# Performance work log

Measured on AMD Instinct MI355X. Metric: run time of the kernel, lower is better.

Reference implementation:

```python
import jax, jax.numpy as jnp
import numpy as np

EMBED_DIM = 1024
NUM_HEADS = 16
HEAD_DIM = EMBED_DIM // NUM_HEADS


def setup_inputs() -> dict:
    key = jax.random.key(0)
    ks = jax.random.split(key, 9)
    B, T, C = 2, 2048, EMBED_DIM
    s = 1.0 / np.sqrt(C)
    return {
        "x": jax.random.normal(ks[0], (B, T, C), dtype=jnp.float32),
        "Wq": jax.random.normal(ks[1], (C, C), dtype=jnp.float32) * s,
        "bq": jnp.zeros((C,), dtype=jnp.float32),
        "Wk": jax.random.normal(ks[2], (C, C), dtype=jnp.float32) * s,
        "bk": jnp.zeros((C,), dtype=jnp.float32),
        "Wv": jax.random.normal(ks[3], (C, C), dtype=jnp.float32) * s,
        "bv": jnp.zeros((C,), dtype=jnp.float32),
        "Wo": jax.random.normal(ks[4], (C, C), dtype=jnp.float32) * s,
        "bo": jnp.zeros((C,), dtype=jnp.float32),
    }


def reference(x, Wq, bq, Wk, bk, Wv, bv, Wo, bo):
    B, T, C = x.shape
    H, D = NUM_HEADS, HEAD_DIM
    # projections (torch Linear: x @ W.T + b; here W stored as [in,out])
    q = (x @ Wq + bq).reshape(B, T, H, D).transpose(0, 2, 1, 3)  # [B,H,T,D]
    k = (x @ Wk + bk).reshape(B, T, H, D).transpose(0, 2, 1, 3)
    v = (x @ Wv + bv).reshape(B, T, H, D).transpose(0, 2, 1, 3)
    scores = jnp.einsum("bhtd,bhsd->bhts", q, k) / jnp.sqrt(jnp.float32(D))
    causal = jnp.tril(jnp.ones((T, T), dtype=bool))  # keep lower triangle
    scores = jnp.where(causal, scores, -jnp.inf)
    weights = jax.nn.softmax(scores, axis=-1)
    attended = jnp.einsum("bhts,bhsd->bhtd", weights, v)
    attended = attended.transpose(0, 2, 1, 3).reshape(B, T, C)
    return attended @ Wo + bo
```

## Files before the change

### kernel.cpp

```cpp
#include <hip/hip_runtime.h>
#include <math.h>


#define BLOCK 256

typedef __attribute__((ext_vector_type(8))) short bf16x8;
typedef __attribute__((ext_vector_type(4))) float f32x4;
typedef __attribute__((ext_vector_type(16))) float f32x16;

__device__ inline short f2bf(float f) {
  union { float f; unsigned u; } c; c.f = f;
  unsigned u = c.u;
  unsigned r = (u + 0x7fffu + ((u >> 16) & 1u)) >> 16;
  return (short)r;
}


__global__ void cvt_all_kernel(const float* __restrict__ x,
                               const float* __restrict__ Wq, const float* __restrict__ Wk,
                               const float* __restrict__ Wv, const float* __restrict__ Wo,
                               short* __restrict__ xb,
                               short* __restrict__ Wtqkv, short* __restrict__ Wto) {
  int z = blockIdx.z;
  if (z >= 4) {
    int blk = blockIdx.x + (blockIdx.y << 5) + ((z - 4) << 10);
    int i = (blk * 256 + threadIdx.x) * 8;
    float4 a = *(const float4*)(x + i);
    float4 b = *(const float4*)(x + i + 4);
    alignas(16) short o[8];
    o[0] = f2bf(a.x); o[1] = f2bf(a.y); o[2] = f2bf(a.z); o[3] = f2bf(a.w);
    o[4] = f2bf(b.x); o[5] = f2bf(b.y); o[6] = f2bf(b.z); o[7] = f2bf(b.w);
    *(int4*)(xb + i) = *(int4*)o;
    return;
  }
  __shared__ float tile[32][33];
  const float* W = (z == 0) ? Wq : (z == 1) ? Wk : (z == 2) ? Wv : Wo;
  short* outp = (z == 3) ? Wto : (Wtqkv + (size_t)z * 1024 * 1024);
  int k0 = blockIdx.x * 32, n0 = blockIdx.y * 32;
  int tr = threadIdx.x >> 5, tc = threadIdx.x & 31;
#pragma unroll
  for (int i = 0; i < 4; i++)
    tile[tr + i * 8][tc] = W[(k0 + tr + i * 8) * 1024 + n0 + tc];
  __syncthreads();
#pragma unroll
  for (int i = 0; i < 4; i++)
    outp[(n0 + tr + i * 8) * 1024 + k0 + tc] = f2bf(tile[tc][tr + i * 8]);
}


__global__ __launch_bounds__(BLOCK, 3) void gemm_qkv_kernel(
    const short* __restrict__ A, const short* __restrict__ Wt,
    const float* __restrict__ bq, const float* __restrict__ bk,
    const float* __restrict__ bv,
    short* __restrict__ Qo, short* __restrict__ Ko, short* __restrict__ Vo) {
  const int Kd = 1024;
  const float QSCL = 0.18033688011f;
  int p = blockIdx.x;
  int xcd = p & 7, j = p >> 3;
  int m0 = ((xcd & 3) * 8 + (j & 7)) * 128;
  int n0 = ((xcd >> 2) * 12 + (j >> 3)) * 128;
  int t = threadIdx.x;
  int lane = t & 63, wv = t >> 6;
  int quad = lane >> 4, lc = lane & 15;
  int wy = wv >> 1, wx = wv & 1;
  __shared__ short As[128 * 64];
  __shared__ short Bs[128 * 64];
  f32x4 acc[4][4] = {};

  int sr = wv * 32 + (lane >> 3);
  int schk = lane & 7;
  const short* Ab = A + (size_t)(m0 + sr) * Kd + schk * 8;
  const short* Bb = Wt + (size_t)(n0 + sr) * Kd + schk * 8;
  int wslot = schk ^ (lane >> 3);
  short* wa = &As[sr * 64 + wslot * 8];
  short* wb = &Bs[sr * 64 + wslot * 8];

  bf16x8 sA[4], sB[4];
#pragma unroll
  for (int i = 0; i < 4; i++) {
    sA[i] = *(const bf16x8*)(Ab + (size_t)(i * 8) * Kd);
    sB[i] = *(const bf16x8*)(Bb + (size_t)(i * 8) * Kd);
  }
  int rx = lc & 7;
  for (int step = 0; step < 16; step++) {
#pragma unroll
    for (int i = 0; i < 4; i++) {
      *(bf16x8*)(wa + i * 8 * 64) = sA[i];
      *(bf16x8*)(wb + i * 8 * 64) = sB[i];
    }
    asm volatile("s_waitcnt lgkmcnt(0)" ::: "memory");
    __builtin_amdgcn_s_barrier();
    asm volatile("" ::: "memory");
    if (step + 1 < 16) {
      int koff = (step + 1) * 64;
#pragma unroll
      for (int i = 0; i < 4; i++) {
        sA[i] = *(const bf16x8*)(Ab + (size_t)(i * 8) * Kd + koff);
        sB[i] = *(const bf16x8*)(Bb + (size_t)(i * 8) * Kd + koff);
      }
    }
#pragma unroll
    for (int kc = 0; kc < 2; kc++) {
      bf16x8 af[4], bf[4];
#pragma unroll
      for (int i = 0; i < 4; i++)
        af[i] = *(const bf16x8*)&As[(wy * 64 + i * 16 + lc) * 64 +
                                    ((kc * 4 + quad) ^ rx) * 8];
#pragma unroll
      for (int i = 0; i < 4; i++)
        bf[i] = *(const bf16x8*)&Bs[(wx * 64 + i * 16 + lc) * 64 +
                                    ((kc * 4 + quad) ^ rx) * 8];
#pragma unroll
      for (int mi = 0; mi < 4; mi++)
#pragma unroll
        for (int ni = 0; ni < 4; ni++)
          acc[mi][ni] = __builtin_amdgcn_mfma_f32_16x16x32_bf16(af[mi], bf[ni], acc[mi][ni], 0, 0, 0);
    }
    asm volatile("s_waitcnt lgkmcnt(0)" ::: "memory");
    __builtin_amdgcn_s_barrier();
    asm volatile("" ::: "memory");
  }
#pragma unroll
  for (int mi = 0; mi < 4; mi++) {
    int row = m0 + wy * 64 + mi * 16 + quad * 4;
#pragma unroll
    for (int ni = 0; ni < 4; ni++) {
      int col = n0 + wx * 64 + ni * 16 + lc;
      int which = col >> 10;
      int hd = col & 1023;
      int h = hd >> 6, d = hd & 63;
      float bb = (which == 0) ? bq[hd] : (which == 1) ? bk[hd] : bv[hd];
      if (which == 2) {
        alignas(8) short pk[4];
#pragma unroll
        for (int r = 0; r < 4; r++) pk[r] = f2bf(acc[mi][ni][r] + bb);
        int b = row >> 11, tt = row & 2047;
        *(int2*)&Vo[((size_t)(b * 16 + h) * 64 + d) * 2048 + tt] = *(const int2*)pk;
      } else {
#pragma unroll
        for (int r = 0; r < 4; r++) {
          int rw = row + r;
          int b = rw >> 11, tt = rw & 2047;
          float val = acc[mi][ni][r] + bb;
          if (which == 0) {
            Qo[((size_t)(b * 16 + h) * 2048 + tt) * 64 + d] = f2bf(val * QSCL);
          } else {
            Ko[((size_t)(b * 16 + h) * 2048 + tt) * 64 + d] = f2bf(val);
          }
        }
      }
    }
  }
}


__global__ __launch_bounds__(BLOCK) void gemm_out_kernel(
    const short* __restrict__ A, const short* __restrict__ Wt,
    const float* __restrict__ bias, float* __restrict__ Out) {
  const int Kd = 1024;
  int m0 = blockIdx.x * 64, n0 = blockIdx.y * 128;
  int t = threadIdx.x;
  int lane = t & 63, wv = t >> 6;
  int quad = lane >> 4, lc = lane & 15;
  int wy = wv >> 1, wx = wv & 1;
  __shared__ short As[64 * 64];
  __shared__ short Bs[128 * 64];
  f32x4 acc[2][4] = {};

  int lr = lane >> 3;
  int schk = lane & 7;
  int wslot = schk ^ lr;
  int srA = wv * 16 + lr;
  int srB = wv * 32 + lr;
  const short* Ab = A + (size_t)(m0 + srA) * Kd + schk * 8;
  const short* Bb = Wt + (size_t)(n0 + srB) * Kd + schk * 8;
  short* wa = &As[srA * 64 + wslot * 8];
  short* wb = &Bs[srB * 64 + wslot * 8];

  bf16x8 sA[2], sB[4];
#pragma unroll
  for (int i = 0; i < 2; i++) sA[i] = *(const bf16x8*)(Ab + (size_t)(i * 8) * Kd);
#pragma unroll
  for (int i = 0; i < 4; i++) sB[i] = *(const bf16x8*)(Bb + (size_t)(i * 8) * Kd);

  int rx = lc & 7;
  for (int step = 0; step < 16; step++) {
#pragma unroll
    for (int i = 0; i < 2; i++) *(bf16x8*)(wa + i * 8 * 64) = sA[i];
#pragma unroll
    for (int i = 0; i < 4; i++) *(bf16x8*)(wb + i * 8 * 64) = sB[i];
    asm volatile("s_waitcnt lgkmcnt(0)" ::: "memory");
    __builtin_amdgcn_s_barrier();
    asm volatile("" ::: "memory");
    if (step + 1 < 16) {
      int koff = (step + 1) * 64;
#pragma unroll
      for (int i = 0; i < 2; i++)
        sA[i] = *(const bf16x8*)(Ab + (size_t)(i * 8) * Kd + koff);
#pragma unroll
      for (int i = 0; i < 4; i++)
        sB[i] = *(const bf16x8*)(Bb + (size_t)(i * 8) * Kd + koff);
    }
#pragma unroll
    for (int kc = 0; kc < 2; kc++) {
      bf16x8 af[2], bf[4];
#pragma unroll
      for (int i = 0; i < 2; i++)
        af[i] = *(const bf16x8*)&As[(wy * 32 + i * 16 + lc) * 64 +
                                    ((kc * 4 + quad) ^ rx) * 8];
#pragma unroll
      for (int i = 0; i < 4; i++)
        bf[i] = *(const bf16x8*)&Bs[(wx * 64 + i * 16 + lc) * 64 +
                                    ((kc * 4 + quad) ^ rx) * 8];
#pragma unroll
      for (int mi = 0; mi < 2; mi++)
#pragma unroll
        for (int ni = 0; ni < 4; ni++)
          acc[mi][ni] = __builtin_amdgcn_mfma_f32_16x16x32_bf16(af[mi], bf[ni], acc[mi][ni], 0, 0, 0);
    }
    asm volatile("s_waitcnt lgkmcnt(0)" ::: "memory");
    __builtin_amdgcn_s_barrier();
    asm volatile("" ::: "memory");
  }
#pragma unroll
  for (int mi = 0; mi < 2; mi++) {
    int row = m0 + wy * 32 + mi * 16 + quad * 4;
#pragma unroll
    for (int ni = 0; ni < 4; ni++) {
      int col = n0 + wx * 64 + ni * 16 + lc;
      float bb = bias[col];
#pragma unroll
      for (int r = 0; r < 4; r++)
        Out[(size_t)(row + r) * 1024 + col] = acc[mi][ni][r] + bb;
    }
  }
}


__global__ __launch_bounds__(BLOCK, 2) void attn_kernel(
    const short* __restrict__ Q, const short* __restrict__ K,
    const short* __restrict__ Vt, short* __restrict__ Oa) {
  int p = blockIdx.x;
  int bh = ((p & 7) << 2) | ((p >> 3) & 3);
  int pair = p >> 5;
  int t = threadIdx.x;
  int lane = t & 63, w = t >> 6;
  int qh = w & 1, kh = w >> 1;
  int ln = lane & 31, lh = lane >> 5;
  const short* Qb = Q + (size_t)bh * 2048 * 64;
  const short* Kb = K + (size_t)bh * 2048 * 64;
  const short* Vg = Vt + (size_t)bh * 64 * 2048;
  int b = bh >> 4, h = bh & 15;

  __shared__ short Kt[128 * 64];
  __shared__ short Vs[64 * 128];
  __shared__ __align__(16) short Ps[4][32 * 72];
  __shared__ float lx[2][64];
  short* Pw = Ps[w];

  int ksr = t >> 3, kchk = t & 7;
  int kslot = (kchk ^ (ksr & 7)) * 8;
  int vsr = t >> 4, vchk = t & 15;
  int vslot = (vchk ^ (vsr & 7)) * 8;

  const float M2 = 14.5f;
  int xk = ln & 7;

  for (int sp = 0; sp < 2; sp++) {
    int s = sp ? (31 - pair) : pair;
    int q0w = s * 64 + qh * 32;
    int qmaxw = q0w + 31;
    int ntiles = (s + 2) >> 1;

    bf16x8 qf[4];
#pragma unroll
    for (int c = 0; c < 4; c++)
      qf[c] = *(const bf16x8*)&Qb[(size_t)(q0w + ln) * 64 + c * 16 + lh * 8];

    f32x16 O0 = {}, O1 = {};
    float lsum = 0.f;

    bf16x8 sK[4], sV[4];
#pragma unroll
    for (int i = 0; i < 4; i++)
      sK[i] = *(const bf16x8*)&Kb[(size_t)(i * 32 + ksr) * 64 + kchk * 8];
#pragma unroll
    for (int i = 0; i < 4; i++)
      sV[i] = *(const bf16x8*)&Vg[(size_t)(i * 16 + vsr) * 2048 + vchk * 8];

    for (int kt = 0; kt < ntiles; kt++) {
#pragma unroll
      for (int i = 0; i < 4; i++)
        *(bf16x8*)&Kt[(i * 32 + ksr) * 64 + kslot] = sK[i];
#pragma unroll
      for (int i = 0; i < 4; i++)
        *(bf16x8*)&Vs[(i * 16 + vsr) * 128 + vslot] = sV[i];
      asm volatile("s_waitcnt lgkmcnt(0)" ::: "memory");
      __builtin_amdgcn_s_barrier();
      asm volatile("" ::: "memory");
      if (kt + 1 < ntiles) {
        int kb2 = (kt + 1) * 128;
#pragma unroll
        for (int i = 0; i < 4; i++)
          sK[i] = *(const bf16x8*)&Kb[(size_t)(kb2 + i * 32 + ksr) * 64 + kchk * 8];
#pragma unroll
        for (int i = 0; i < 4; i++)
          sV[i] = *(const bf16x8*)&Vg[(size_t)(i * 16 + vsr) * 2048 + kb2 + vchk * 8];
      }
#pragma unroll
      for (int kg = 0; kg < 2; kg++) {
        int grpbase = kt * 128 + kh * 64 + kg * 32;
        if (grpbase <= qmaxw) {
          f32x16 S = {};
#pragma unroll
          for (int c = 0; c < 4; c++) {
            int ch = c * 2 + lh;
            bf16x8 kf = *(const bf16x8*)&Kt[(kh * 64 + kg * 32 + ln) * 64 + (ch ^ xk) * 8];
            S = __builtin_amdgcn_mfma_f32_32x32x16_bf16(kf, qf[c], S, 0, 0, 0);
          }
          if (grpbase + 31 > q0w) {
            int qg = q0w + ln;
#pragma unroll
            for (int reg = 0; reg < 16; reg++) {
              int key = grpbase + (reg & 3) + 8 * (reg >> 2) + 4 * lh;
              if (key > qg) S[reg] = -3.0e38f;
            }
          }
#pragma unroll
          for (int g = 0; g < 4; g++) {
            unsigned u[4];
            float e[4];
#pragma unroll
            for (int i = 0; i < 4; i++) {
              union { float f; unsigned v; } cc;
              cc.f = __builtin_amdgcn_exp2f(S[g * 4 + i] - M2);
              e[i] = cc.f;
              u[i] = cc.v + 0x8000u;
            }
            lsum += (e[0] + e[1]) + (e[2] + e[3]);
            int2 pk;
            pk.x = (int)__builtin_amdgcn_perm(u[1], u[0], 0x07060302);
            pk.y = (int)__builtin_amdgcn_perm(u[3], u[2], 0x07060302);
            *(int2*)&Pw[ln * 72 + kg * 32 + g * 8 + lh * 4] = pk;
          }
#pragma unroll
          for (int cc = 0; cc < 2; cc++) {
            bf16x8 pf = *(const bf16x8*)&Pw[ln * 72 + kg * 32 + cc * 16 + lh * 8];
            int ch = kh * 8 + kg * 4 + cc * 2 + lh;
            bf16x8 v0 = *(const bf16x8*)&Vs[ln * 128 + (ch ^ xk) * 8];
            bf16x8 v1 = *(const bf16x8*)&Vs[(32 + ln) * 128 + (ch ^ xk) * 8];
            O0 = __builtin_amdgcn_mfma_f32_32x32x16_bf16(v0, pf, O0, 0, 0, 0);
            O1 = __builtin_amdgcn_mfma_f32_32x32x16_bf16(v1, pf, O1, 0, 0, 0);
          }
        }
      }
      asm volatile("s_waitcnt lgkmcnt(0)" ::: "memory");
      __builtin_amdgcn_s_barrier();
      asm volatile("" ::: "memory");
    }

    float* ob = (float*)&Ps[0][0];
    if (kh == 1) {
      float* obw = ob + qh * 2048;
#pragma unroll
      for (int dh = 0; dh < 2; dh++)
#pragma unroll
        for (int reg = 0; reg < 16; reg++)
          obw[((dh * 16 + reg) * 2 + lh) * 32 + ln] = dh ? O1[reg] : O0[reg];
      lx[qh][lane] = lsum;
    }
    __syncthreads();
    if (kh == 0) {
      float* obw = ob + qh * 2048;
#pragma unroll
      for (int reg = 0; reg < 16; reg++) {
        O0[reg] += obw[((0 * 16 + reg) * 2 + lh) * 32 + ln];
        O1[reg] += obw[((1 * 16 + reg) * 2 + lh) * 32 + ln];
      }
      float lt = lsum + lx[qh][lane];
      lt += __shfl_xor(lt, 32, 64);
      float inv = 1.0f / lt;
      size_t rowbase = (size_t)(b * 2048 + q0w + ln) * 1024 + h * 64;
#pragma unroll
      for (int dh = 0; dh < 2; dh++)
#pragma unroll
        for (int g = 0; g < 4; g++) {
          alignas(8) short pk[4];
#pragma unroll
          for (int i = 0; i < 4; i++) {
            float v = dh ? O1[g * 4 + i] : O0[g * 4 + i];
            pk[i] = f2bf(v * inv);
          }
          *(int2*)&Oa[rowbase + dh * 32 + g * 8 + lh * 4] = *(const int2*)pk;
        }
    }
  }
}


extern "C" void kernel_launch(void* const* d_in, const int* in_sizes, int n_in,
                              void* d_out, int out_size, void* d_ws, size_t ws_size,
                              hipStream_t stream) {
  const float* x = (const float*)d_in[0];
  const float* Wq = (const float*)d_in[1];
  const float* bq = (const float*)d_in[2];
  const float* Wk = (const float*)d_in[3];
  const float* bk = (const float*)d_in[4];
  const float* Wv = (const float*)d_in[5];
  const float* bv = (const float*)d_in[6];
  const float* Wo = (const float*)d_in[7];
  const float* bo = (const float*)d_in[8];
  char* ws = (char*)d_ws;
  const size_t MB = 1024 * 1024;
  short* xb = (short*)(ws);
  short* Wtqkv = (short*)(ws + 8 * MB);
  short* Wto = (short*)(ws + 14 * MB);
  short* Qb = (short*)(ws + 17 * MB);
  short* Kb = (short*)(ws + 25 * MB);
  short* Vb = (short*)(ws + 33 * MB);
  short* Att = (short*)(ws + 41 * MB);
  float* out = (float*)d_out;

  cvt_all_kernel<<<dim3(32, 32, 6), BLOCK, 0, stream>>>(x, Wq, Wk, Wv, Wo, xb, Wtqkv, Wto);
  gemm_qkv_kernel<<<dim3(768), BLOCK, 0, stream>>>(xb, Wtqkv, bq, bk, bv, Qb, Kb, Vb);
  attn_kernel<<<512, BLOCK, 0, stream>>>(Qb, Kb, Vb, Att);
  gemm_out_kernel<<<dim3(64, 8), BLOCK, 0, stream>>>(Att, Wto, bo, out);
}
```

Measured before the change: 172.8 us.

## Split attention work across four key-wave groups per 32-row query tile

Each block now handles a 32-row query tile, with all four waves splitting the 128-key tile into 32-key slices, instead of two query halves times two key halves. The grid doubles to 1024 blocks with paired causal tiles, and launch bounds rise to 3 blocks per CU. This aims for better load balance and occupancy. The cost is a four-way reduction of partial outputs through LDS reused from K/V buffers, an extra barrier per pass, and K/V tiles loaded once per 32 query rows rather than 64, which doubles K/V traffic.

```diff
diff --git a/kernel.cpp b/kernel.cpp
--- a/kernel.cpp
+++ b/kernel.cpp
@@ -237,15 +237,14 @@
 }
 
 
-__global__ __launch_bounds__(BLOCK, 2) void attn_kernel(
+__global__ __launch_bounds__(BLOCK, 3) void attn_kernel(
     const short* __restrict__ Q, const short* __restrict__ K,
     const short* __restrict__ Vt, short* __restrict__ Oa) {
   int p = blockIdx.x;
   int bh = ((p & 7) << 2) | ((p >> 3) & 3);
   int pair = p >> 5;
   int t = threadIdx.x;
-  int lane = t & 63, w = t >> 6;
-  int qh = w & 1, kh = w >> 1;
+  int lane = t & 63, kh = t >> 6;
   int ln = lane & 31, lh = lane >> 5;
   const short* Qb = Q + (size_t)bh * 2048 * 64;
   const short* Kb = K + (size_t)bh * 2048 * 64;
@@ -254,9 +253,9 @@
 
   __shared__ short Kt[128 * 64];
   __shared__ short Vs[64 * 128];
-  __shared__ __align__(16) short Ps[4][32 * 72];
-  __shared__ float lx[2][64];
-  short* Pw = Ps[w];
+  __shared__ __align__(16) short Ps[4][32 * 40];
+  __shared__ float lx[4][64];
+  short* Pw = Ps[kh];
 
   int ksr = t >> 3, kchk = t & 7;
   int kslot = (kchk ^ (ksr & 7)) * 8;
@@ -267,10 +266,10 @@
   int xk = ln & 7;
 
   for (int sp = 0; sp < 2; sp++) {
-    int s = sp ? (31 - pair) : pair;
-    int q0w = s * 64 + qh * 32;
+    int s = sp ? (63 - pair) : pair;
+    int q0w = s * 32;
     int qmaxw = q0w + 31;
-    int ntiles = (s + 2) >> 1;
+    int ntiles = (s >> 2) + 1;
 
     bf16x8 qf[4];
 #pragma unroll
@@ -307,51 +306,48 @@
         for (int i = 0; i < 4; i++)
           sV[i] = *(const bf16x8*)&Vg[(size_t)(i * 16 + vsr) * 2048 + kb2 + vchk * 8];
       }
-#pragma unroll
-      for (int kg = 0; kg < 2; kg++) {
-        int grpbase = kt * 128 + kh * 64 + kg * 32;
-        if (grpbase <= qmaxw) {
-          f32x16 S = {};
-#pragma unroll
-          for (int c = 0; c < 4; c++) {
-            int ch = c * 2 + lh;
-            bf16x8 kf = *(const bf16x8*)&Kt[(kh * 64 + kg * 32 + ln) * 64 + (ch ^ xk) * 8];
-            S = __builtin_amdgcn_mfma_f32_32x32x16_bf16(kf, qf[c], S, 0, 0, 0);
+      int grpbase = kt * 128 + kh * 32;
+      if (grpbase <= qmaxw) {
+        f32x16 S = {};
+#pragma unroll
+        for (int c = 0; c < 4; c++) {
+          int ch = c * 2 + lh;
+          bf16x8 kf = *(const bf16x8*)&Kt[(kh * 32 + ln) * 64 + (ch ^ xk) * 8];
+          S = __builtin_amdgcn_mfma_f32_32x32x16_bf16(kf, qf[c], S, 0, 0, 0);
+        }
+        if (grpbase >= q0w) {
+          int qg = q0w + ln;
+#pragma unroll
+          for (int reg = 0; reg < 16; reg++) {
+            int key = grpbase + (reg & 3) + 8 * (reg >> 2) + 4 * lh;
+            if (key > qg) S[reg] = -3.0e38f;
           }
-          if (grpbase + 31 > q0w) {
-            int qg = q0w + ln;
-#pragma unroll
-            for (int reg = 0; reg < 16; reg++) {
-              int key = grpbase + (reg & 3) + 8 * (reg >> 2) + 4 * lh;
-              if (key > qg) S[reg] = -3.0e38f;
-            }
+        }
+#pragma unroll
+        for (int g = 0; g < 4; g++) {
+          unsigned u[4];
+          float e[4];
+#pragma unroll
+          for (int i = 0; i < 4; i++) {
+            union { float f; unsigned v; } cc;
+            cc.f = __builtin_amdgcn_exp2f(S[g * 4 + i] - M2);
+            e[i] = cc.f;
+            u[i] = cc.v + 0x8000u;
           }
-#pragma unroll
-          for (int g = 0; g < 4; g++) {
-            unsigned u[4];
-            float e[4];
-#pragma unroll
-            for (int i = 0; i < 4; i++) {
-              union { float f; unsigned v; } cc;
-              cc.f = __builtin_amdgcn_exp2f(S[g * 4 + i] - M2);
-              e[i] = cc.f;
-              u[i] = cc.v + 0x8000u;
-            }
-            lsum += (e[0] + e[1]) + (e[2] + e[3]);
-            int2 pk;
-            pk.x = (int)__builtin_amdgcn_perm(u[1], u[0], 0x07060302);
-            pk.y = (int)__builtin_amdgcn_perm(u[3], u[2], 0x07060302);
-            *(int2*)&Pw[ln * 72 + kg * 32 + g * 8 + lh * 4] = pk;
-          }
-#pragma unroll
-          for (int cc = 0; cc < 2; cc++) {
-            bf16x8 pf = *(const bf16x8*)&Pw[ln * 72 + kg * 32 + cc * 16 + lh * 8];
-            int ch = kh * 8 + kg * 4 + cc * 2 + lh;
-            bf16x8 v0 = *(const bf16x8*)&Vs[ln * 128 + (ch ^ xk) * 8];
-            bf16x8 v1 = *(const bf16x8*)&Vs[(32 + ln) * 128 + (ch ^ xk) * 8];
-            O0 = __builtin_amdgcn_mfma_f32_32x32x16_bf16(v0, pf, O0, 0, 0, 0);
-            O1 = __builtin_amdgcn_mfma_f32_32x32x16_bf16(v1, pf, O1, 0, 0, 0);
-          }
+          lsum += (e[0] + e[1]) + (e[2] + e[3]);
+          int2 pk;
+          pk.x = (int)__builtin_amdgcn_perm(u[1], u[0], 0x07060302);
+          pk.y = (int)__builtin_amdgcn_perm(u[3], u[2], 0x07060302);
+          *(int2*)&Pw[ln * 40 + g * 8 + lh * 4] = pk;
+        }
+#pragma unroll
+        for (int cc = 0; cc < 2; cc++) {
+          bf16x8 pf = *(const bf16x8*)&Pw[ln * 40 + cc * 16 + lh * 8];
+          int ch = kh * 4 + cc * 2 + lh;
+          bf16x8 v0 = *(const bf16x8*)&Vs[ln * 128 + (ch ^ xk) * 8];
+          bf16x8 v1 = *(const bf16x8*)&Vs[(32 + ln) * 128 + (ch ^ xk) * 8];
+          O0 = __builtin_amdgcn_mfma_f32_32x32x16_bf16(v0, pf, O0, 0, 0, 0);
+          O1 = __builtin_amdgcn_mfma_f32_32x32x16_bf16(v1, pf, O1, 0, 0, 0);
         }
       }
       asm volatile("s_waitcnt lgkmcnt(0)" ::: "memory");
@@ -359,25 +355,28 @@
       asm volatile("" ::: "memory");
     }
 
-    float* ob = (float*)&Ps[0][0];
-    if (kh == 1) {
-      float* obw = ob + qh * 2048;
+    float* R0 = (float*)&Kt[0];
+    float* R1 = (float*)&Kt[0] + 2048;
+    float* R2 = (float*)&Vs[0];
+    lx[kh][lane] = lsum;
+    if (kh != 0) {
+      float* Rw = (kh == 1) ? R0 : (kh == 2) ? R1 : R2;
 #pragma unroll
       for (int dh = 0; dh < 2; dh++)
 #pragma unroll
         for (int reg = 0; reg < 16; reg++)
-          obw[((dh * 16 + reg) * 2 + lh) * 32 + ln] = dh ? O1[reg] : O0[reg];
-      lx[qh][lane] = lsum;
+          Rw[((dh * 16 + reg) * 2 + lh) * 32 + ln] = dh ? O1[reg] : O0[reg];
     }
     __syncthreads();
     if (kh == 0) {
-      float* obw = ob + qh * 2048;
 #pragma unroll
       for (int reg = 0; reg < 16; reg++) {
-        O0[reg] += obw[((0 * 16 + reg) * 2 + lh) * 32 + ln];
-        O1[reg] += obw[((1 * 16 + reg) * 2 + lh) * 32 + ln];
+        int i0 = ((0 * 16 + reg) * 2 + lh) * 32 + ln;
+        int i1 = ((1 * 16 + reg) * 2 + lh) * 32 + ln;
+        O0[reg] += (R0[i0] + R1[i0]) + R2[i0];
+        O1[reg] += (R0[i1] + R1[i1]) + R2[i1];
       }
-      float lt = lsum + lx[qh][lane];
+      float lt = lsum + ((lx[1][lane] + lx[2][lane]) + lx[3][lane]);
       lt += __shfl_xor(lt, 32, 64);
       float inv = 1.0f / lt;
       size_t rowbase = (size_t)(b * 2048 + q0w + ln) * 1024 + h * 64;
@@ -394,6 +393,7 @@
           *(int2*)&Oa[rowbase + dh * 32 + g * 8 + lh * 4] = *(const int2*)pk;
         }
     }
+    __syncthreads();
   }
 }
 
@@ -423,6 +423,6 @@
 
   cvt_all_kernel<<<dim3(32, 32, 6), BLOCK, 0, stream>>>(x, Wq, Wk, Wv, Wo, xb, Wtqkv, Wto);
   gemm_qkv_kernel<<<dim3(768), BLOCK, 0, stream>>>(xb, Wtqkv, bq, bk, bv, Qb, Kb, Vb);
-  attn_kernel<<<512, BLOCK, 0, stream>>>(Qb, Kb, Vb, Att);
+  attn_kernel<<<1024, BLOCK, 0, stream>>>(Qb, Kb, Vb, Att);
   gemm_out_kernel<<<dim3(64, 8), BLOCK, 0, stream>>>(Att, Wto, bo, out);
 }
```

After: 190.6 us. 1.1x slower.
